# Kernel optimization log

Measured on AMD Instinct MI355X. Metric: run time of the kernel, lower is better.

The kernel has to match this reference:

```python
import jax, jax.numpy as jnp
import numpy as np

NUM_HEADS = 16
HEAD_DIM = 64
D_MODEL = NUM_HEADS * HEAD_DIM  # 1024
TOP_K_TILES = 8
TILE_SIZE = 16


def setup_inputs() -> dict:
    key = jax.random.key(0)
    kx, kq, kk, kv, ko = jax.random.split(key, 5)
    B, S = 2, 2048
    scale = 1.0 / np.sqrt(D_MODEL)
    return {
        "x": jax.random.normal(kx, (B, S, D_MODEL), dtype=jnp.float32),
        "wq": jax.random.normal(kq, (D_MODEL, NUM_HEADS * HEAD_DIM), dtype=jnp.float32) * scale,
        "wk": jax.random.normal(kk, (D_MODEL, NUM_HEADS * HEAD_DIM), dtype=jnp.float32) * scale,
        "wv": jax.random.normal(kv, (D_MODEL, NUM_HEADS * HEAD_DIM), dtype=jnp.float32) * scale,
        "wo": jax.random.normal(ko, (NUM_HEADS * HEAD_DIM, D_MODEL), dtype=jnp.float32) * scale,
    }


def reference(x, wq, wk, wv, wo):
    B, S, _ = x.shape
    H, D = NUM_HEADS, HEAD_DIM
    q = (x @ wq).reshape(B, S, H, D)
    k = (x @ wk).reshape(B, S, H, D)
    v = (x @ wv).reshape(B, S, H, D)
    logits = jnp.einsum('bqhd,bkhd->bhqk', q, k) / jnp.sqrt(jnp.float32(D))
    causal = jnp.tril(jnp.ones((S, S), dtype=bool))
    logits = jnp.where(causal[None, None, :, :], logits, jnp.float32(-1e10))
    weights = jax.nn.softmax(logits, axis=-1)  # [B,H,S,S]

    # tile pooling + top-k on the last query row (auxiliary output, cached in original)
    last_token_probs = weights[:, :, -1, :]  # [B,H,S]
    pad_len = (TILE_SIZE - S % TILE_SIZE) % TILE_SIZE
    if pad_len > 0:
        last_token_probs = jnp.pad(last_token_probs, ((0, 0), (0, 0), (0, pad_len)))
    num_tiles = last_token_probs.shape[-1] // TILE_SIZE
    tile_scores = last_token_probs.reshape(B, H, num_tiles, TILE_SIZE).max(axis=-1)
    _, top_tile_indices = jax.lax.top_k(tile_scores, TOP_K_TILES)  # side output
    del top_tile_indices  # original stores in a global cache; not returned

    out = jnp.einsum('bhqk,bkhd->bqhd', weights, v).reshape(B, S, H * D)
    return out @ wo
```

## Files before the change

kernel.cpp:

```cpp
#include <hip/hip_runtime.h>
#include <hip/hip_bf16.h>

#define NUM_HEADS 16
#define HEAD_DIM 64
#define DMODEL 1024
#define SEQ 2048
#define BATCH 2
#define MROWS (BATCH*SEQ)

typedef __bf16 bf16;
typedef __bf16 bf16x4 __attribute__((ext_vector_type(4)));
typedef __bf16 bf16x8 __attribute__((ext_vector_type(8)));
typedef float f32x4 __attribute__((ext_vector_type(4)));

#define MFMA16(a, b, c) __builtin_amdgcn_mfma_f32_16x16x32_bf16((a), (b), (c), 0, 0, 0)

#define QSCALE 0.1803368801111444f

__device__ __forceinline__ float fast_exp2(float x) {
    float r;
    asm("v_exp_f32 %0, %1" : "=v"(r) : "v"(x));
    return r;
}

__device__ __forceinline__ void gld16(const void* g, void* l) {
    __builtin_amdgcn_global_load_lds(
        (const __attribute__((address_space(1))) void*)g,
        (__attribute__((address_space(3))) void*)l, 16, 0, 0);
}


__global__ __launch_bounds__(256) void cvt_f32_bf16(const float* __restrict__ in,
                                                    bf16* __restrict__ out, int n4) {
    int i = blockIdx.x * 256 + threadIdx.x;
    if (i >= n4) return;
    float4 v = *(const float4*)(in + (size_t)i * 4);
    bf16x4 o = { (bf16)v.x, (bf16)v.y, (bf16)v.z, (bf16)v.w };
    *(bf16x4*)(out + (size_t)i * 4) = o;
}

__global__ __launch_bounds__(256) void cvt_trans(const float* __restrict__ w0, const float* __restrict__ w1,
                                                 const float* __restrict__ w2, const float* __restrict__ w3,
                                                 bf16* __restrict__ o0, bf16* __restrict__ o1,
                                                 bf16* __restrict__ o2, bf16* __restrict__ o3) {
    const float* w = blockIdx.z == 0 ? w0 : blockIdx.z == 1 ? w1 : blockIdx.z == 2 ? w2 : w3;
    bf16* o = blockIdx.z == 0 ? o0 : blockIdx.z == 1 ? o1 : blockIdx.z == 2 ? o2 : o3;
    __shared__ bf16 tile[64][65];
    int k0 = blockIdx.y * 64, n0 = blockIdx.x * 64;
    int tc = threadIdx.x & 63;
    int tr0 = threadIdx.x >> 6;
#pragma unroll
    for (int i = 0; i < 16; i++) {
        int r = tr0 + i * 4;
        tile[r][tc] = (bf16)w[(size_t)(k0 + r) * DMODEL + n0 + tc];
    }
    __syncthreads();
#pragma unroll
    for (int i = 0; i < 16; i++) {
        int r = tr0 + i * 4;
        o[(size_t)(n0 + r) * DMODEL + k0 + tc] = tile[tc][r];
    }
}


#define BM 128
#define BN 128
#define BK 32

__device__ __forceinline__ void gemm_core(const bf16* __restrict__ A, const bf16* __restrict__ Bt,
                                          int m0, int n0, int Kdim,
                                          bf16* As, bf16* Bs, f32x4 acc[4][4]) {
    int t = threadIdx.x;
    int lane = t & 63;
    int wave = t >> 6;
    int wm = (wave >> 1) * 64;
    int wn = (wave & 1) * 64;
#pragma unroll
    for (int mf = 0; mf < 4; mf++)
#pragma unroll
        for (int nf = 0; nf < 4; nf++) acc[mf][nf] = (f32x4){0.f, 0.f, 0.f, 0.f};

    int arow = lane & 15, kg = lane >> 4;

    for (int k0 = 0; k0 < Kdim; k0 += BK) {
        __syncthreads();
#pragma unroll
        for (int it = 0; it < 2; it++) {
            int chunk = it * 256 + t;
            int rr = chunk >> 2, cc = chunk & 3;
            gld16(A + (size_t)(m0 + rr) * Kdim + k0 + cc * 8, As + chunk * 8);
            gld16(Bt + (size_t)(n0 + rr) * Kdim + k0 + cc * 8, Bs + chunk * 8);
        }
        __syncthreads();
        bf16x8 af[4], bfr[4];
#pragma unroll
        for (int mf = 0; mf < 4; mf++)
            af[mf] = *(const bf16x8*)(As + (wm + mf * 16 + arow) * BK + kg * 8);
#pragma unroll
        for (int nf = 0; nf < 4; nf++)
            bfr[nf] = *(const bf16x8*)(Bs + (wn + nf * 16 + arow) * BK + kg * 8);
#pragma unroll
        for (int mf = 0; mf < 4; mf++)
#pragma unroll
            for (int nf = 0; nf < 4; nf++)
                acc[mf][nf] = MFMA16(af[mf], bfr[nf], acc[mf][nf]);
    }
}

__global__ __launch_bounds__(256) void gemm_qkv(const bf16* __restrict__ xb,
                                                const bf16* __restrict__ wqT, const bf16* __restrict__ wkT,
                                                const bf16* __restrict__ wvT,
                                                bf16* __restrict__ Qh, bf16* __restrict__ Kh,
                                                bf16* __restrict__ Vt) {
    __shared__ __attribute__((aligned(16))) bf16 As[BM * BK];
    __shared__ __attribute__((aligned(16))) bf16 Bs[BN * BK];
    int z = blockIdx.z;
    const bf16* Bt = z == 0 ? wqT : z == 1 ? wkT : wvT;
    int m0 = blockIdx.y * BM, n0 = blockIdx.x * BN;
    f32x4 acc[4][4];
    gemm_core(xb, Bt, m0, n0, DMODEL, As, Bs, acc);

    int lane = threadIdx.x & 63, wave = threadIdx.x >> 6;
    int wm = (wave >> 1) * 64, wn = (wave & 1) * 64;
    int col0 = n0 + wn + (lane & 15);
    int row0 = m0 + wm + (lane >> 4) * 4;
    if (z < 2) {
        bf16* O = z == 0 ? Qh : Kh;
        float scl = z == 0 ? QSCALE : 1.0f;
#pragma unroll
        for (int mf = 0; mf < 4; mf++)
#pragma unroll
            for (int nf = 0; nf < 4; nf++) {
                int n = col0 + nf * 16;
                int mb = row0 + mf * 16;
                int hh = n >> 6, d = n & 63;
#pragma unroll
                for (int i2 = 0; i2 < 4; i2++) {
                    int m = mb + i2;
                    int bb = m >> 11, s = m & 2047;
                    O[(((size_t)bb * NUM_HEADS + hh) * SEQ + s) * HEAD_DIM + d] =
                        (bf16)(acc[mf][nf][i2] * scl);
                }
            }
    } else {
#pragma unroll
        for (int mf = 0; mf < 4; mf++)
#pragma unroll
            for (int nf = 0; nf < 4; nf++) {
                int n = col0 + nf * 16;
                int m = row0 + mf * 16;
                int b = m >> 11, s = m & 2047;
                int h = n >> 6, d = n & 63;
                bf16x4 pack = { (bf16)acc[mf][nf][0], (bf16)acc[mf][nf][1],
                                (bf16)acc[mf][nf][2], (bf16)acc[mf][nf][3] };
                *(bf16x4*)(Vt + ((size_t)(b * NUM_HEADS + h) * HEAD_DIM + d) * SEQ + s) = pack;
            }
    }
}

__global__ __launch_bounds__(256) void gemm_outp(const bf16* __restrict__ at,
                                                 const bf16* __restrict__ woT,
                                                 float* __restrict__ out) {
    __shared__ __attribute__((aligned(16))) bf16 As[BM * BK];
    __shared__ __attribute__((aligned(16))) bf16 Bs[BN * BK];
    int m0 = blockIdx.y * BM, n0 = blockIdx.x * BN;
    f32x4 acc[4][4];
    gemm_core(at, woT, m0, n0, DMODEL, As, Bs, acc);

    int lane = threadIdx.x & 63, wave = threadIdx.x >> 6;
    int wm = (wave >> 1) * 64, wn = (wave & 1) * 64;
    int col0 = n0 + wn + (lane & 15);
    int row0 = m0 + wm + (lane >> 4) * 4;
#pragma unroll
    for (int mf = 0; mf < 4; mf++)
#pragma unroll
        for (int nf = 0; nf < 4; nf++) {
            int n = col0 + nf * 16;
            int mb = row0 + mf * 16;
#pragma unroll
            for (int i2 = 0; i2 < 4; i2++)
                out[(size_t)(mb + i2) * DMODEL + n] = acc[mf][nf][i2];
        }
}

__global__ __launch_bounds__(256) void attn_kernel(const bf16* __restrict__ Qh, const bf16* __restrict__ Kh,
                                                   const bf16* __restrict__ Vt, bf16* __restrict__ attn) {
    __shared__ __attribute__((aligned(16))) bf16 Kl[2 * 64 * 64];
    __shared__ __attribute__((aligned(16))) bf16 Vl[2 * 64 * 64];
    __shared__ __attribute__((aligned(16))) bf16 Pl[4 * 16 * 64];
    int id = blockIdx.x;
    int xcd = id & 7, slot = id >> 3;
    int bh4 = slot >> 4;
    int pairIdx = slot & 15;
    int hb = xcd * 4 + bh4;
    int b = hb >> 4, h = hb & 15;
    int t = threadIdx.x, lane = t & 63, wave = t >> 6;
    int l15 = lane & 15, lg = lane >> 4;

    const bf16* Qb = Qh + ((size_t)(b * NUM_HEADS + h) * SEQ) * HEAD_DIM;
    const bf16* Kb = Kh + ((size_t)(b * NUM_HEADS + h) * SEQ) * HEAD_DIM;
    const bf16* Vb = Vt + ((size_t)(b * NUM_HEADS + h) * HEAD_DIM) * SEQ;

    char* Pw = (char*)Pl + wave * 2048;
    int swz = (l15 & 7) << 4;

    auto STAGE = [&](int bufi, int kv0n) {
#pragma unroll
        for (int j = 0; j < 2; j++) {
            int c = j * 256 + t;
            int L = (c * 16) ^ (((c >> 3) & 7) << 4);
            int row = c >> 3, cole = (L & 127) >> 1;
            gld16(Kb + (size_t)(kv0n + row) * HEAD_DIM + cole,
                  (char*)Kl + (size_t)bufi * 8192 + c * 16);
            gld16(Vb + (size_t)row * SEQ + kv0n + cole,
                  (char*)Vl + (size_t)bufi * 8192 + c * 16);
        }
    };

#pragma unroll 1
    for (int seg = 0; seg < 2; seg++) {
        int qt = seg ? (31 - pairIdx) : pairIdx;
        int q0w = qt * 64 + wave * 16;
        int nkt = qt + 1;

        bf16x8 qf[2];
#pragma unroll
        for (int ks = 0; ks < 2; ks++)
            qf[ks] = *(const bf16x8*)(Qb + (size_t)(q0w + l15) * HEAD_DIM + ks * 32 + lg * 8);

        f32x4 oacc[4];
#pragma unroll
        for (int df = 0; df < 4; df++) oacc[df] = (f32x4){0.f, 0.f, 0.f, 0.f};
        float mrun = -1e30f, lrun = 0.f;

        STAGE(0, 0);
        __syncthreads();
        int buf = 0;

        for (int kt = 0; kt < nkt; kt++) {
            int kv0 = kt * 64;
            if (kt + 1 < nkt) STAGE(buf ^ 1, kv0 + 64);

            const char* KL = (const char*)Kl + (size_t)buf * 8192;
            const char* VL = (const char*)Vl + (size_t)buf * 8192;
            f32x4 st[4];
            __builtin_amdgcn_s_setprio(1);
#pragma unroll
            for (int cf = 0; cf < 4; cf++) {
                bf16x8 kfr[2];
#pragma unroll
                for (int ks = 0; ks < 2; ks++) {
                    int off = ((cf * 16 + l15) * 128 + ks * 64 + lg * 16) ^ swz;
                    kfr[ks] = *(const bf16x8*)(KL + off);
                }
                st[cf] = (f32x4){0.f, 0.f, 0.f, 0.f};
#pragma unroll
                for (int ks = 0; ks < 2; ks++)
                    st[cf] = MFMA16(kfr[ks], qf[ks], st[cf]);
            }
            __builtin_amdgcn_s_setprio(0);
            if (kt == nkt - 1) {
                int qrow = q0w + l15;
#pragma unroll
                for (int cf = 0; cf < 4; cf++)
#pragma unroll
                    for (int i = 0; i < 4; i++) {
                        int kv = kv0 + cf * 16 + lg * 4 + i;
                        if (kv > qrow) st[cf][i] = -1e30f;
                    }
            }
            float m01 = fmaxf(fmaxf(st[0][0], st[0][1]), fmaxf(st[0][2], st[0][3]));
            float m23 = fmaxf(fmaxf(st[1][0], st[1][1]), fmaxf(st[1][2], st[1][3]));
            float m45 = fmaxf(fmaxf(st[2][0], st[2][1]), fmaxf(st[2][2], st[2][3]));
            float m67 = fmaxf(fmaxf(st[3][0], st[3][1]), fmaxf(st[3][2], st[3][3]));
            float mx = fmaxf(fmaxf(m01, m23), fmaxf(m45, m67));
            mx = fmaxf(mx, __shfl_xor(mx, 16, 64));
            mx = fmaxf(mx, __shfl_xor(mx, 32, 64));
            if (!__all(mx <= mrun + 8.0f)) {
                float mnew = fmaxf(mrun, mx);
                float alpha = fast_exp2(mrun - mnew);
                float av[4];
#pragma unroll
                for (int i = 0; i < 4; i++) av[i] = __shfl(alpha, lg * 4 + i, 64);
#pragma unroll
                for (int df = 0; df < 4; df++)
#pragma unroll
                    for (int i = 0; i < 4; i++) oacc[df][i] *= av[i];
                lrun *= alpha;
                mrun = mnew;
            }
            float psc[4];
            bf16x4 pb[4];
#pragma unroll
            for (int cf = 0; cf < 4; cf++) {
                float p0 = fast_exp2(st[cf][0] - mrun);
                float p1 = fast_exp2(st[cf][1] - mrun);
                float p2 = fast_exp2(st[cf][2] - mrun);
                float p3 = fast_exp2(st[cf][3] - mrun);
                psc[cf] = (p0 + p1) + (p2 + p3);
                pb[cf][0] = (bf16)p0; pb[cf][1] = (bf16)p1;
                pb[cf][2] = (bf16)p2; pb[cf][3] = (bf16)p3;
            }
            float ps = (psc[0] + psc[1]) + (psc[2] + psc[3]);
            ps += __shfl_xor(ps, 16, 64);
            ps += __shfl_xor(ps, 32, 64);
            lrun += ps;
#pragma unroll
            for (int cf = 0; cf < 4; cf++) {
                int off = (l15 * 128 + cf * 32 + lg * 8) ^ swz;
                *(bf16x4*)(Pw + off) = pb[cf];
            }
            bf16x8 pa[2];
#pragma unroll
            for (int ks = 0; ks < 2; ks++) {
                int off = (l15 * 128 + ks * 64 + lg * 16) ^ swz;
                pa[ks] = *(const bf16x8*)(Pw + off);
            }
            __builtin_amdgcn_s_setprio(1);
#pragma unroll
            for (int ks = 0; ks < 2; ks++)
#pragma unroll
                for (int df = 0; df < 4; df++) {
                    int off = ((df * 16 + l15) * 128 + ks * 64 + lg * 16) ^ swz;
                    bf16x8 bv = *(const bf16x8*)(VL + off);
                    oacc[df] = MFMA16(pa[ks], bv, oacc[df]);
                }
            __builtin_amdgcn_s_setprio(0);

            __syncthreads();
            buf ^= 1;
        }

        float lrec = 1.0f / lrun;
        float lv[4];
#pragma unroll
        for (int i = 0; i < 4; i++) lv[i] = __shfl(lrec, lg * 4 + i, 64);
#pragma unroll
        for (int df = 0; df < 4; df++)
#pragma unroll
            for (int i = 0; i < 4; i++) {
                int qrow = q0w + lg * 4 + i;
                int d = df * 16 + l15;
                attn[((size_t)(b * SEQ + qrow)) * DMODEL + h * HEAD_DIM + d] = (bf16)(oacc[df][i] * lv[i]);
            }
    }
}


extern "C" void kernel_launch(void* const* d_in, const int* in_sizes, int n_in,
                              void* d_out, int out_size, void* d_ws, size_t ws_size,
                              hipStream_t stream) {
    const float* x  = (const float*)d_in[0];
    const float* wq = (const float*)d_in[1];
    const float* wk = (const float*)d_in[2];
    const float* wv = (const float*)d_in[3];
    const float* wo = (const float*)d_in[4];
    float* out = (float*)d_out;

    char* w = (char*)d_ws;
    bf16* xb  = (bf16*)(w);
    bf16* wqT = (bf16*)(w + (8ull  << 20));
    bf16* wkT = (bf16*)(w + (10ull << 20));
    bf16* wvT = (bf16*)(w + (12ull << 20));
    bf16* woT = (bf16*)(w + (14ull << 20));
    bf16* Qh  = (bf16*)(w + (16ull << 20));
    bf16* Kh  = (bf16*)(w + (24ull << 20));
    bf16* Vt  = (bf16*)(w + (32ull << 20));
    bf16* at  = (bf16*)(w + (40ull << 20));

    cvt_f32_bf16<<<(MROWS * DMODEL / 4 + 255) / 256, 256, 0, stream>>>(x, xb, MROWS * DMODEL / 4);
    cvt_trans<<<dim3(16, 16, 4), 256, 0, stream>>>(wq, wk, wv, wo, wqT, wkT, wvT, woT);
    gemm_qkv<<<dim3(DMODEL / BN, MROWS / BM, 3), 256, 0, stream>>>(xb, wqT, wkT, wvT, Qh, Kh, Vt);
    attn_kernel<<<dim3(512, 1, 1), 256, 0, stream>>>(Qh, Kh, Vt, at);
    gemm_outp<<<dim3(DMODEL / BN, MROWS / BM), 256, 0, stream>>>(at, woT, out);
}
```

Measured before the change: 119.1 us.

## Fuse conversion kernels, remap GEMM tiles per XCD, simplify attention buffer indexing

Merges the x conversion and weight transpose-conversion into a single launch, removing one kernel launch and its inter-kernel gap. Remaps GEMM block indices so each XCD works on contiguous row blocks and shares more of A in its L2. Also restructures the attention double-buffer indexing to derive the buffer from kt and adds unroll 1 on the KV loop, which mostly cleans up the code and may change register use.

```diff
diff --git a/kernel.cpp b/kernel.cpp
--- a/kernel.cpp
+++ b/kernel.cpp
@@ -29,36 +29,39 @@
         (__attribute__((address_space(3))) void*)l, 16, 0, 0);
 }
 
-
-__global__ __launch_bounds__(256) void cvt_f32_bf16(const float* __restrict__ in,
-                                                    bf16* __restrict__ out, int n4) {
-    int i = blockIdx.x * 256 + threadIdx.x;
-    if (i >= n4) return;
-    float4 v = *(const float4*)(in + (size_t)i * 4);
-    bf16x4 o = { (bf16)v.x, (bf16)v.y, (bf16)v.z, (bf16)v.w };
-    *(bf16x4*)(out + (size_t)i * 4) = o;
-}
-
-__global__ __launch_bounds__(256) void cvt_trans(const float* __restrict__ w0, const float* __restrict__ w1,
-                                                 const float* __restrict__ w2, const float* __restrict__ w3,
-                                                 bf16* __restrict__ o0, bf16* __restrict__ o1,
-                                                 bf16* __restrict__ o2, bf16* __restrict__ o3) {
-    const float* w = blockIdx.z == 0 ? w0 : blockIdx.z == 1 ? w1 : blockIdx.z == 2 ? w2 : w3;
-    bf16* o = blockIdx.z == 0 ? o0 : blockIdx.z == 1 ? o1 : blockIdx.z == 2 ? o2 : o3;
+__global__ __launch_bounds__(256) void cvt_all(const float* __restrict__ x,
+                                               const float* __restrict__ w0, const float* __restrict__ w1,
+                                               const float* __restrict__ w2, const float* __restrict__ w3,
+                                               bf16* __restrict__ xb,
+                                               bf16* __restrict__ o0, bf16* __restrict__ o1,
+                                               bf16* __restrict__ o2, bf16* __restrict__ o3) {
     __shared__ bf16 tile[64][65];
-    int k0 = blockIdx.y * 64, n0 = blockIdx.x * 64;
+    int id = blockIdx.x;
+    if (id < 4096) {
+        int i = id * 256 + threadIdx.x;
+        float4 v = *(const float4*)(x + (size_t)i * 4);
+        bf16x4 o = { (bf16)v.x, (bf16)v.y, (bf16)v.z, (bf16)v.w };
+        *(bf16x4*)(xb + (size_t)i * 4) = o;
+        return;
+    }
+    id -= 4096;
+    int z = id >> 8, r = id & 255;
+    int by = r >> 4, bx = r & 15;
+    const float* w = z == 0 ? w0 : z == 1 ? w1 : z == 2 ? w2 : w3;
+    bf16* o = z == 0 ? o0 : z == 1 ? o1 : z == 2 ? o2 : o3;
+    int k0 = by * 64, n0 = bx * 64;
     int tc = threadIdx.x & 63;
     int tr0 = threadIdx.x >> 6;
 #pragma unroll
     for (int i = 0; i < 16; i++) {
-        int r = tr0 + i * 4;
-        tile[r][tc] = (bf16)w[(size_t)(k0 + r) * DMODEL + n0 + tc];
+        int rr = tr0 + i * 4;
+        tile[rr][tc] = (bf16)w[(size_t)(k0 + rr) * DMODEL + n0 + tc];
     }
     __syncthreads();
 #pragma unroll
     for (int i = 0; i < 16; i++) {
-        int r = tr0 + i * 4;
-        o[(size_t)(n0 + r) * DMODEL + k0 + tc] = tile[tc][r];
+        int rr = tr0 + i * 4;
+        o[(size_t)(n0 + rr) * DMODEL + k0 + tc] = tile[tc][rr];
     }
 }
 
@@ -105,6 +108,13 @@
             for (int nf = 0; nf < 4; nf++)
                 acc[mf][nf] = MFMA16(af[mf], bfr[nf], acc[mf][nf]);
     }
+}
+
+__device__ __forceinline__ void xcd_remap(int bx, int by, int& m0, int& n0) {
+    int f = bx + 8 * by;
+    int xcd = f & 7, k = f >> 3;
+    m0 = (xcd * 4 + (k & 3)) * BM;
+    n0 = (k >> 2) * BN;
 }
 
 __global__ __launch_bounds__(256) void gemm_qkv(const bf16* __restrict__ xb,
@@ -116,7 +126,8 @@
     __shared__ __attribute__((aligned(16))) bf16 Bs[BN * BK];
     int z = blockIdx.z;
     const bf16* Bt = z == 0 ? wqT : z == 1 ? wkT : wvT;
-    int m0 = blockIdx.y * BM, n0 = blockIdx.x * BN;
+    int m0, n0;
+    xcd_remap(blockIdx.x, blockIdx.y, m0, n0);
     f32x4 acc[4][4];
     gemm_core(xb, Bt, m0, n0, DMODEL, As, Bs, acc);
 
@@ -163,7 +174,8 @@
                                                  float* __restrict__ out) {
     __shared__ __attribute__((aligned(16))) bf16 As[BM * BK];
     __shared__ __attribute__((aligned(16))) bf16 Bs[BN * BK];
-    int m0 = blockIdx.y * BM, n0 = blockIdx.x * BN;
+    int m0, n0;
+    xcd_remap(blockIdx.x, blockIdx.y, m0, n0);
     f32x4 acc[4][4];
     gemm_core(at, woT, m0, n0, DMODEL, As, Bs, acc);
 
@@ -204,16 +216,15 @@
     char* Pw = (char*)Pl + wave * 2048;
     int swz = (l15 & 7) << 4;
 
-    auto STAGE = [&](int bufi, int kv0n) {
+    auto STAGE = [&](int kt) {
+        int kv0n = kt * 64, bi = kt & 1;
 #pragma unroll
         for (int j = 0; j < 2; j++) {
             int c = j * 256 + t;
             int L = (c * 16) ^ (((c >> 3) & 7) << 4);
             int row = c >> 3, cole = (L & 127) >> 1;
-            gld16(Kb + (size_t)(kv0n + row) * HEAD_DIM + cole,
-                  (char*)Kl + (size_t)bufi * 8192 + c * 16);
-            gld16(Vb + (size_t)row * SEQ + kv0n + cole,
-                  (char*)Vl + (size_t)bufi * 8192 + c * 16);
+            gld16(Kb + (size_t)(kv0n + row) * HEAD_DIM + cole, (char*)Kl + bi * 8192 + c * 16);
+            gld16(Vb + (size_t)row * SEQ + kv0n + cole,        (char*)Vl + bi * 8192 + c * 16);
         }
     };
 
@@ -233,16 +244,16 @@
         for (int df = 0; df < 4; df++) oacc[df] = (f32x4){0.f, 0.f, 0.f, 0.f};
         float mrun = -1e30f, lrun = 0.f;
 
-        STAGE(0, 0);
+        STAGE(0);
         __syncthreads();
-        int buf = 0;
-
+
+#pragma unroll 1
         for (int kt = 0; kt < nkt; kt++) {
+            if (kt + 1 < nkt) STAGE(kt + 1);
+
             int kv0 = kt * 64;
-            if (kt + 1 < nkt) STAGE(buf ^ 1, kv0 + 64);
-
-            const char* KL = (const char*)Kl + (size_t)buf * 8192;
-            const char* VL = (const char*)Vl + (size_t)buf * 8192;
+            const char* KL = (const char*)Kl + (kt & 1) * 8192;
+            const char* VL = (const char*)Vl + (kt & 1) * 8192;
             f32x4 st[4];
             __builtin_amdgcn_s_setprio(1);
 #pragma unroll
@@ -328,7 +339,6 @@
             __builtin_amdgcn_s_setprio(0);
 
             __syncthreads();
-            buf ^= 1;
         }
 
         float lrec = 1.0f / lrun;
@@ -368,8 +378,7 @@
     bf16* Vt  = (bf16*)(w + (32ull << 20));
     bf16* at  = (bf16*)(w + (40ull << 20));
 
-    cvt_f32_bf16<<<(MROWS * DMODEL / 4 + 255) / 256, 256, 0, stream>>>(x, xb, MROWS * DMODEL / 4);
-    cvt_trans<<<dim3(16, 16, 4), 256, 0, stream>>>(wq, wk, wv, wo, wqT, wkT, wvT, woT);
+    cvt_all<<<5120, 256, 0, stream>>>(x, wq, wk, wv, wo, xb, wqT, wkT, wvT, woT);
     gemm_qkv<<<dim3(DMODEL / BN, MROWS / BM, 3), 256, 0, stream>>>(xb, wqT, wkT, wvT, Qh, Kh, Vt);
     attn_kernel<<<dim3(512, 1, 1), 256, 0, stream>>>(Qh, Kh, Vt, at);
     gemm_outp<<<dim3(DMODEL / BN, MROWS / BM), 256, 0, stream>>>(at, woT, out);
```

After: 116.9 us. Within noise of the previous version (-1.8%).
